# Kernel tuning notes

Measured on AMD Instinct MI355X. Metric: run time of the kernel, lower is better.

Reference implementation:

```python
import jax, jax.numpy as jnp
import numpy as np

RANK = 8
A_SHAPE = (64, 128)   # (a1, a2)
B_SHAPE = (16, 32)    # (b1, b2)
BATCH = 16384


def setup_inputs() -> dict:
    key = jax.random.key(0)
    k1, k2, k3, k4, k5 = jax.random.split(key, 5)
    a1, a2 = A_SHAPE
    b1, b2 = B_SHAPE
    x = jax.random.normal(k1, (BATCH, a1 * b1), dtype=jnp.float32)
    # xavier-uniform style init for a and b (as in nn.init.xavier_uniform_)
    lim_a = float(np.sqrt(6.0 / (a1 + a2)))
    lim_b = float(np.sqrt(6.0 / (b1 + b2)))
    a = jax.random.uniform(k2, (RANK, a1, a2), minval=-lim_a, maxval=lim_a, dtype=jnp.float32)
    b = jax.random.uniform(k3, (RANK, b1, b2), minval=-lim_b, maxval=lim_b, dtype=jnp.float32)
    s = jax.random.normal(k4, (a1, a2), dtype=jnp.float32)          # structured-sparse mask
    bias = jax.random.normal(k5, (a2 * b2,), dtype=jnp.float32)     # bias_shape[1:] = (a2*b2,)
    return {"x": x, "a": a, "b": b, "s": s, "bias": bias}


def reference(x, a, b, s, bias):
    # structured-sparse elementwise mask on a
    a_eff = s[None, :, :] * a                          # (rank, a1, a2)
    r, a1, a2 = a_eff.shape
    _, b1, b2 = b.shape
    # w = sum_r kron(a_eff[r], b[r]) : (a1*b1, a2*b2)
    w = jnp.einsum('rij,rkl->ikjl', a_eff, b).reshape(a1 * b1, a2 * b2)
    out = x @ w                                        # (batch, a2*b2)
    return out + bias[None, :]
```

## Files before the change

### kernel.cpp

```cpp
#include <hip/hip_runtime.h>
#include <hip/hip_bf16.h>

typedef short bf16x8 __attribute__((ext_vector_type(8)));
typedef float f32x4 __attribute__((ext_vector_type(4)));

static constexpr int M_DIM = 16384;
static constexpr int N_DIM = 4096;
static constexpr int K_DIM = 1024;

static constexpr int CVT_BLOCKS = (M_DIM * K_DIM / 8) / 256;
static constexpr int WT_BLOCKS  = 128;

__device__ __forceinline__ unsigned short f2bf(float f) {
  union { float f; unsigned u; } v; v.f = f;
  unsigned r = v.u + 0x7FFFu + ((v.u >> 16) & 1u);
  return (unsigned short)(r >> 16);
}

__global__ __launch_bounds__(256) void prep_kernel(
    const float* __restrict__ x, const float* __restrict__ a,
    const float* __restrict__ b, const float* __restrict__ s,
    unsigned short* __restrict__ xb, unsigned short* __restrict__ wT) {
  const int tid = threadIdx.x;

  if (blockIdx.x < CVT_BLOCKS) {
    const int i = (blockIdx.x * 256 + tid) * 2;
    float4 v0 = reinterpret_cast<const float4*>(x)[i];
    float4 v1 = reinterpret_cast<const float4*>(x)[i + 1];
    ushort4 o0, o1;
    o0.x = f2bf(v0.x); o0.y = f2bf(v0.y); o0.z = f2bf(v0.z); o0.w = f2bf(v0.w);
    o1.x = f2bf(v1.x); o1.y = f2bf(v1.y); o1.z = f2bf(v1.z); o1.w = f2bf(v1.w);
    reinterpret_cast<ushort4*>(xb)[i] = o0;
    reinterpret_cast<ushort4*>(xb)[i + 1] = o1;
    return;
  }

  __shared__ float as_eff[8][64];
  __shared__ float bsh[8][16][32];
  const int j = blockIdx.x - CVT_BLOCKS;

#pragma unroll
  for (int t = tid; t < 4096; t += 256)
    ((float*)bsh)[t] = b[t];
#pragma unroll
  for (int t = tid; t < 512; t += 256) {
    const int r = t >> 6, i = t & 63;
    as_eff[r][i] = a[(r * 64 + i) * 128 + j] * s[i * 128 + j];
  }
  __syncthreads();

  const int i = tid >> 2;
  const int kk0 = (tid & 3) * 4;
  float av[8];
#pragma unroll
  for (int r = 0; r < 8; ++r) av[r] = as_eff[r][i];

#pragma unroll 4
  for (int l = 0; l < 32; ++l) {
    float o[4] = {0.f, 0.f, 0.f, 0.f};
#pragma unroll
    for (int r = 0; r < 8; ++r)
#pragma unroll
      for (int q = 0; q < 4; ++q)
        o[q] += av[r] * bsh[r][kk0 + q][l];
    ushort4 w4;
    w4.x = f2bf(o[0]); w4.y = f2bf(o[1]); w4.z = f2bf(o[2]); w4.w = f2bf(o[3]);
    *reinterpret_cast<ushort4*>(&wT[(size_t)(j * 32 + l) * K_DIM + tid * 4]) = w4;
  }
}


#define PH_BARRIER __builtin_amdgcn_s_barrier()
#define SCHED0     __builtin_amdgcn_sched_barrier(0)
#define WAITV(N)   do { asm volatile("s_waitcnt vmcnt(" #N ")" ::: "memory"); SCHED0; } while (0)
#define WAITL(N)   do { asm volatile("s_waitcnt lgkmcnt(" #N ")" ::: "memory"); SCHED0; } while (0)

__device__ __forceinline__ void quad_mfma(f32x4 (&acc)[8][4], const bf16x8 (&aH)[4][2],
                                          const bf16x8 (&bH)[2][2], int mbase, int nbase) {
  __builtin_amdgcn_s_setprio(1);
#pragma unroll
  for (int ks = 0; ks < 2; ++ks)
#pragma unroll
    for (int mi = 0; mi < 4; ++mi)
#pragma unroll
      for (int ni = 0; ni < 2; ++ni)
        acc[mbase + mi][nbase + ni] = __builtin_amdgcn_mfma_f32_16x16x32_bf16(
            aH[mi][ks], bH[ni][ks], acc[mbase + mi][nbase + ni], 0, 0, 0);
  __builtin_amdgcn_s_setprio(0);
}

__global__ __launch_bounds__(512, 2) void gemm8_kernel(
    const unsigned short* __restrict__ A, const unsigned short* __restrict__ BT,
    const float* __restrict__ bias, float* __restrict__ C) {
  __shared__ __align__(16) unsigned short Al[2][16384];
  __shared__ __align__(16) unsigned short Bl[3][16384];

  const int tid  = threadIdx.x;
  const int lane = tid & 63;
  const int wave = tid >> 6;
  const int wm = wave >> 2;
  const int wn = wave & 3;
  const int wr = wm * 128;
  const int wc = wn * 64;
  const int frow = lane & 15;
  const int kg = lane >> 4;
  const int swz0 = (kg * 16) ^ ((lane & 7) << 4);
  const int swz1 = (64 + kg * 16) ^ ((lane & 7) << 4);

  int bid = blockIdx.x;
  int gid = bid >> 4, lid = bid & 15;
  gid = ((gid & 7) << 3) | (gid >> 3);
  const int bm = (gid >> 2) * 4 + (lid >> 2);
  const int bn = (gid & 3) * 4 + (lid & 3);
  const int brow = bm * 256, bcol = bn * 256;

  const unsigned short* Abase = A + (size_t)brow * K_DIM;
  const unsigned short* Bbase = BT + (size_t)bcol * K_DIM;

  const int srow = tid >> 3;
  const int scol = ((((tid & 7) << 4) ^ ((srow & 7) << 4)) >> 1);
  const int ldsu = __builtin_amdgcn_readfirstlane(wave * 512);

#define STG(dst, base, q, k0) __builtin_amdgcn_global_load_lds( \
    (const __attribute__((address_space(1))) void*)((base) + (size_t)((q)*64 + srow) * K_DIM + (k0) + scol), \
    (__attribute__((address_space(3))) void*)((dst) + (q)*4096 + ldsu), 16, 0, 0)

#define STG4(dst, base, k0) do { STG(dst, base, 0, k0); STG(dst, base, 1, k0); \
                                 STG(dst, base, 2, k0); STG(dst, base, 3, k0); } while (0)

#define LOAD_AH(P, h) { _Pragma("unroll") for (int mi = 0; mi < 4; ++mi) { \
    const char* p_ = (const char*)(P) + (wr + frow + ((h)*4 + mi) * 16) * 128; \
    aF[mi][0] = *(const bf16x8*)(p_ + swz0); aF[mi][1] = *(const bf16x8*)(p_ + swz1); } }

#define LOAD_BH(P, h, dst) { _Pragma("unroll") for (int ni = 0; ni < 2; ++ni) { \
    const char* p_ = (const char*)(P) + (wc + frow + ((h)*2 + ni) * 16) * 128; \
    dst[ni][0] = *(const bf16x8*)(p_ + swz0); dst[ni][1] = *(const bf16x8*)(p_ + swz1); } }

  f32x4 acc[8][4] = {};
  bf16x8 aF[4][2], b0[2][2], b1[2][2];

  STG4(Bl[0], Bbase, 0);
  STG4(Al[0], Abase, 0);
  STG4(Bl[1], Bbase, 64);
  WAITV(4);
  PH_BARRIER;

  unsigned short* a_rd = &Al[0][0]; unsigned short* a_st = &Al[1][0];
  unsigned short* b_rd = &Bl[0][0]; unsigned short* b_nx = &Bl[1][0];
  unsigned short* b_st = &Bl[2][0];

#pragma unroll 1
  for (int t = 0; t < 16; ++t) {
    const int k = t * 64;
    LOAD_AH(a_rd, 0); SCHED0;
    LOAD_BH(b_rd, 0, b0); SCHED0;
    LOAD_BH(b_rd, 1, b1); SCHED0;
    if (t < 15) STG4(a_st, Abase, k + 64);
    if (t < 14) STG4(b_st, Bbase, k + 128);
    WAITL(4);
    quad_mfma(acc, aF, b0, 0, 0);
    WAITL(0);
    quad_mfma(acc, aF, b1, 0, 2);
    LOAD_AH(a_rd, 1); SCHED0;
    WAITL(0);
    quad_mfma(acc, aF, b1, 4, 2);
    quad_mfma(acc, aF, b0, 4, 0);
    if (t < 14) { WAITV(4); } else { WAITV(0); }
    PH_BARRIER;
    unsigned short* ta = a_rd; a_rd = a_st; a_st = ta;
    unsigned short* tb = b_rd; b_rd = b_nx; b_nx = b_st; b_st = tb;
  }

  __syncthreads();
  float* T = (float*)&Al[0][0];
  float* Tw = T + wave * (16 * 68);
  const int col4 = lane & 15;
  const int rsel = lane >> 4;
  float4 bv = *(const float4*)&bias[bcol + wc + col4 * 4];

#pragma unroll
  for (int mi = 0; mi < 8; ++mi) {
#pragma unroll
    for (int ni = 0; ni < 4; ++ni)
#pragma unroll
      for (int r = 0; r < 4; ++r)
        Tw[(kg * 4 + r) * 68 + ni * 16 + frow] = acc[mi][ni][r];
    WAITL(0);
#pragma unroll
    for (int rr = 0; rr < 4; ++rr) {
      float4 v = *(float4*)&Tw[(rr * 4 + rsel) * 68 + col4 * 4];
      v.x += bv.x; v.y += bv.y; v.z += bv.z; v.w += bv.w;
      *(float4*)&C[(size_t)(brow + wr + mi * 16 + rr * 4 + rsel) * N_DIM + bcol + wc + col4 * 4] = v;
    }
    WAITL(0);
  }
}

extern "C" void kernel_launch(void* const* d_in, const int* in_sizes, int n_in,
                              void* d_out, int out_size, void* d_ws, size_t ws_size,
                              hipStream_t stream) {
  const float* x    = (const float*)d_in[0];
  const float* a    = (const float*)d_in[1];
  const float* b    = (const float*)d_in[2];
  const float* s    = (const float*)d_in[3];
  const float* bias = (const float*)d_in[4];
  float* out = (float*)d_out;

  unsigned short* xb = (unsigned short*)d_ws;
  unsigned short* wT = (unsigned short*)((char*)d_ws + (size_t)M_DIM * K_DIM * 2);

  prep_kernel<<<CVT_BLOCKS + WT_BLOCKS, 256, 0, stream>>>(x, a, b, s, xb, wT);
  gemm8_kernel<<<(M_DIM / 256) * (N_DIM / 256), 512, 0, stream>>>(xb, wT, bias, out);
}
```

Measured before the change: 195.7 us.

## Interleave split global-to-LDS stages with MFMA phases and parallelize weight prep

The GEMM main loop drops B from triple to double LDS buffering. Each tile load is split into per-quarter async global-to-LDS copies that sit between the MFMA quads, with barriers between phases so the copies overwrite the buffer only after every wave has read it. This spreads memory issue across the compute phases and cuts LDS use, but adds many workgroup barriers per K step. The weight-build part of the prep kernel now uses one block per output column instead of one block per 32 columns, which raises parallelism but repeats the masked-a loads in every block.

```diff
diff --git a/kernel.cpp b/kernel.cpp
--- a/kernel.cpp
+++ b/kernel.cpp
@@ -9,7 +9,7 @@
 static constexpr int K_DIM = 1024;
 
 static constexpr int CVT_BLOCKS = (M_DIM * K_DIM / 8) / 256;
-static constexpr int WT_BLOCKS  = 128;
+static constexpr int WT_BLOCKS  = N_DIM;
 
 __device__ __forceinline__ unsigned short f2bf(float f) {
   union { float f; unsigned u; } v; v.f = f;
@@ -21,6 +21,8 @@
     const float* __restrict__ x, const float* __restrict__ a,
     const float* __restrict__ b, const float* __restrict__ s,
     unsigned short* __restrict__ xb, unsigned short* __restrict__ wT) {
+  __shared__ float as_eff[8][64];
+  __shared__ float bl[8][16];
   const int tid = threadIdx.x;
 
   if (blockIdx.x < CVT_BLOCKS) {
@@ -35,38 +37,33 @@
     return;
   }
 
-  __shared__ float as_eff[8][64];
-  __shared__ float bsh[8][16][32];
-  const int j = blockIdx.x - CVT_BLOCKS;
-
-#pragma unroll
-  for (int t = tid; t < 4096; t += 256)
-    ((float*)bsh)[t] = b[t];
+  const int n = blockIdx.x - CVT_BLOCKS;
+  const int j = n >> 5, l = n & 31;
+
 #pragma unroll
   for (int t = tid; t < 512; t += 256) {
     const int r = t >> 6, i = t & 63;
     as_eff[r][i] = a[(r * 64 + i) * 128 + j] * s[i * 128 + j];
   }
+  if (tid < 128) {
+    const int r = tid >> 4, kk = tid & 15;
+    bl[r][kk] = b[(r * 16 + kk) * 32 + l];
+  }
   __syncthreads();
 
   const int i = tid >> 2;
   const int kk0 = (tid & 3) * 4;
-  float av[8];
-#pragma unroll
-  for (int r = 0; r < 8; ++r) av[r] = as_eff[r][i];
-
-#pragma unroll 4
-  for (int l = 0; l < 32; ++l) {
-    float o[4] = {0.f, 0.f, 0.f, 0.f};
-#pragma unroll
-    for (int r = 0; r < 8; ++r)
-#pragma unroll
-      for (int q = 0; q < 4; ++q)
-        o[q] += av[r] * bsh[r][kk0 + q][l];
-    ushort4 w4;
-    w4.x = f2bf(o[0]); w4.y = f2bf(o[1]); w4.z = f2bf(o[2]); w4.w = f2bf(o[3]);
-    *reinterpret_cast<ushort4*>(&wT[(size_t)(j * 32 + l) * K_DIM + tid * 4]) = w4;
-  }
+  float o[4] = {0.f, 0.f, 0.f, 0.f};
+#pragma unroll
+  for (int r = 0; r < 8; ++r) {
+    const float av = as_eff[r][i];
+#pragma unroll
+    for (int q = 0; q < 4; ++q)
+      o[q] += av * bl[r][kk0 + q];
+  }
+  ushort4 w4;
+  w4.x = f2bf(o[0]); w4.y = f2bf(o[1]); w4.z = f2bf(o[2]); w4.w = f2bf(o[3]);
+  *reinterpret_cast<ushort4*>(&wT[(size_t)n * K_DIM + tid * 4]) = w4;
 }
 
 
@@ -93,7 +90,7 @@
     const unsigned short* __restrict__ A, const unsigned short* __restrict__ BT,
     const float* __restrict__ bias, float* __restrict__ C) {
   __shared__ __align__(16) unsigned short Al[2][16384];
-  __shared__ __align__(16) unsigned short Bl[3][16384];
+  __shared__ __align__(16) unsigned short Bl[2][16384];
 
   const int tid  = threadIdx.x;
   const int lane = tid & 63;
@@ -125,9 +122,6 @@
     (const __attribute__((address_space(1))) void*)((base) + (size_t)((q)*64 + srow) * K_DIM + (k0) + scol), \
     (__attribute__((address_space(3))) void*)((dst) + (q)*4096 + ldsu), 16, 0, 0)
 
-#define STG4(dst, base, k0) do { STG(dst, base, 0, k0); STG(dst, base, 1, k0); \
-                                 STG(dst, base, 2, k0); STG(dst, base, 3, k0); } while (0)
-
 #define LOAD_AH(P, h) { _Pragma("unroll") for (int mi = 0; mi < 4; ++mi) { \
     const char* p_ = (const char*)(P) + (wr + frow + ((h)*4 + mi) * 16) * 128; \
     aF[mi][0] = *(const bf16x8*)(p_ + swz0); aF[mi][1] = *(const bf16x8*)(p_ + swz1); } }
@@ -139,36 +133,48 @@
   f32x4 acc[8][4] = {};
   bf16x8 aF[4][2], b0[2][2], b1[2][2];
 
-  STG4(Bl[0], Bbase, 0);
-  STG4(Al[0], Abase, 0);
-  STG4(Bl[1], Bbase, 64);
+  STG(Bl[0], Bbase, 0, 0);  STG(Bl[0], Bbase, 1, 0);
+  STG(Bl[0], Bbase, 2, 0);  STG(Bl[0], Bbase, 3, 0);
+  STG(Al[0], Abase, 0, 0);  STG(Al[0], Abase, 1, 0);
+  STG(Al[0], Abase, 2, 0);  STG(Al[0], Abase, 3, 0);
+  STG(Bl[1], Bbase, 0, 64); STG(Bl[1], Bbase, 1, 64);
+  STG(Bl[1], Bbase, 2, 64); STG(Bl[1], Bbase, 3, 64);
   WAITV(4);
   PH_BARRIER;
 
   unsigned short* a_rd = &Al[0][0]; unsigned short* a_st = &Al[1][0];
-  unsigned short* b_rd = &Bl[0][0]; unsigned short* b_nx = &Bl[1][0];
-  unsigned short* b_st = &Bl[2][0];
+  unsigned short* b_rd = &Bl[0][0]; unsigned short* b_st = &Bl[1][0];
 
 #pragma unroll 1
   for (int t = 0; t < 16; ++t) {
     const int k = t * 64;
     LOAD_AH(a_rd, 0); SCHED0;
     LOAD_BH(b_rd, 0, b0); SCHED0;
+    if (t < 15) { STG(a_st, Abase, 0, k + 64); STG(a_st, Abase, 1, k + 64); }
+    WAITL(8);
+    PH_BARRIER;
+    WAITL(0);
+    quad_mfma(acc, aF, b0, 0, 0);
+    PH_BARRIER;
     LOAD_BH(b_rd, 1, b1); SCHED0;
-    if (t < 15) STG4(a_st, Abase, k + 64);
-    if (t < 14) STG4(b_st, Bbase, k + 128);
-    WAITL(4);
-    quad_mfma(acc, aF, b0, 0, 0);
+    if (t < 15) { STG(a_st, Abase, 2, k + 64); STG(a_st, Abase, 3, k + 64); }
+    PH_BARRIER;
     WAITL(0);
     quad_mfma(acc, aF, b1, 0, 2);
+    PH_BARRIER;
     LOAD_AH(a_rd, 1); SCHED0;
+    if (t < 14) { STG(b_rd, Bbase, 0, k + 128); STG(b_rd, Bbase, 1, k + 128); }
+    PH_BARRIER;
     WAITL(0);
     quad_mfma(acc, aF, b1, 4, 2);
+    PH_BARRIER;
+    if (t < 14) { STG(b_rd, Bbase, 2, k + 128); STG(b_rd, Bbase, 3, k + 128); }
+    PH_BARRIER;
     quad_mfma(acc, aF, b0, 4, 0);
-    if (t < 14) { WAITV(4); } else { WAITV(0); }
-    PH_BARRIER;
-    unsigned short* ta = a_rd; a_rd = a_st; a_st = ta;
-    unsigned short* tb = b_rd; b_rd = b_nx; b_nx = b_st; b_st = tb;
+    if (t < 14) { WAITV(4); } else if (t == 14) { WAITV(0); }
+    PH_BARRIER;
+    unsigned short* tp = a_rd; a_rd = a_st; a_st = tp;
+    tp = b_rd; b_rd = b_st; b_st = tp;
   }
 
   __syncthreads();
```

After: 188.1 us. -3.9%, faster.
